# Kernel tuning notes

Measured on AMD Instinct MI355X. Metric: run time of the kernel, lower is better.

## Reference

```python
import jax, jax.numpy as jnp
import numpy as np


def setup_inputs() -> dict:
    key = jax.random.key(0)
    ks = jax.random.split(key, 8)
    B, C, H, W = 4, 512, 64, 64
    M = C // 8
    sq = 1.0 / np.sqrt(C)
    return {
        "x": jax.random.normal(ks[0], (B, C, H, W), jnp.float32),
        "Wq": jax.random.normal(ks[1], (M, C), jnp.float32) * sq,
        "bq": jnp.zeros((M,), jnp.float32),
        "Wk": jax.random.normal(ks[2], (M, C), jnp.float32) * sq,
        "bk": jnp.zeros((M,), jnp.float32),
        "Wv": jax.random.normal(ks[3], (C, C), jnp.float32) * sq,
        "bv": jnp.zeros((C,), jnp.float32),
        "gamma": jax.random.uniform(ks[4], (1,), jnp.float32),
    }


def reference(x, Wq, bq, Wk, bk, Wv, bv, gamma):
    B, C, H, W = x.shape
    N = H * W
    xf = x.reshape(B, C, N)  # flatten spatial -> [B, C, N]
    # 1x1 convs are channel-mixing matmuls
    q = jnp.einsum('mc,bcn->bmn', Wq, xf) + bq[None, :, None]  # [B, M, N]
    k = jnp.einsum('mc,bcn->bmn', Wk, xf) + bk[None, :, None]  # [B, M, N]
    v = jnp.einsum('dc,bcn->bdn', Wv, xf) + bv[None, :, None]  # [B, C, N]
    # sim[b,i,j] = <q[:, i], k[:, j]>, softmax over j
    sim = jnp.einsum('bmi,bmj->bij', q, k)  # [B, N, N]
    attn = jax.nn.softmax(sim, axis=-1)
    # feat[b,c,i] = sum_j v[b,c,j] * attn[b,i,j]
    feat = jnp.einsum('bcj,bij->bci', v, attn)  # [B, C, N]
    out = gamma[0] * feat.reshape(B, C, H, W) + x
    return out
```

## Files before the change

### kernel.cpp

```cpp
#include <hip/hip_runtime.h>

typedef _Float16 f16;
typedef _Float16 f16x8 __attribute__((ext_vector_type(8)));
typedef float    f32x4 __attribute__((ext_vector_type(4)));
typedef unsigned int u32x2 __attribute__((ext_vector_type(2)));

#define B_ 4
#define C_ 512
#define N_ 4096
#define M_ 64

#define LGKM_BARRIER()                                        \
    __builtin_amdgcn_sched_barrier(0);                        \
    asm volatile("s_waitcnt lgkmcnt(0)");                     \
    __builtin_amdgcn_s_barrier();                             \
    __builtin_amdgcn_sched_barrier(0);

__device__ __forceinline__ unsigned pk2(float a, float b) {
    union { f16 h[2]; unsigned u; } t;
    t.h[0] = (f16)a; t.h[1] = (f16)b;
    return t.u;
}

__global__ __launch_bounds__(256) void wcvt(
    const float* __restrict__ Wq, const float* __restrict__ Wk,
    const float* __restrict__ Wv, f16* __restrict__ Wf)
{
    const int e = (blockIdx.x * 256 + threadIdx.x) * 8;
    const float* src;
    int off;
    if (e < 32768)      { src = Wq; off = e; }
    else if (e < 65536) { src = Wk; off = e - 32768; }
    else                { src = Wv; off = e - 65536; }
    float4 a = *(const float4*)(src + off);
    float4 b = *(const float4*)(src + off + 4);
    f16x8 o;
    o[0]=(f16)a.x; o[1]=(f16)a.y; o[2]=(f16)a.z; o[3]=(f16)a.w;
    o[4]=(f16)b.x; o[5]=(f16)b.y; o[6]=(f16)b.z; o[7]=(f16)b.w;
    *(f16x8*)(Wf + e) = o;
}

__global__ __launch_bounds__(512, 2) void qkv4(
    const f16* __restrict__ Wf, const float* __restrict__ x,
    const float* __restrict__ bq, const float* __restrict__ bk,
    const float* __restrict__ bv,
    f16* __restrict__ qt, f16* __restrict__ ktf, f16* __restrict__ vf)
{
    __shared__ __align__(16) char sH[3][8192];
    __shared__ float sBias[640];

    const int tid  = threadIdx.x;
    const int w    = tid >> 6;
    const int lane = tid & 63;
    const int l15  = lane & 15;
    const int quad = lane >> 4;
    const int n0   = blockIdx.x * 64;
    const int b    = blockIdx.y;
    const int row0 = w * 80;

    for (int e = tid; e < 640; e += 512)
        sBias[e] = (e < 64) ? bq[e] : (e < 128) ? bk[e - 64] : bv[e - 128];

    const int wbyte = (lane * 128 + w * 16) ^ ((lane & 7) << 4);
    int rbyte[4][2];
    #pragma unroll
    for (int nt = 0; nt < 4; ++nt)
        #pragma unroll
        for (int kh = 0; kh < 2; ++kh)
            rbyte[nt][kh] = ((nt * 16 + l15) * 128 + kh * 64 + quad * 16)
                            ^ ((l15 & 7) << 4);

    const float* xg = x + (size_t)b * (C_ * N_) + n0 + lane;
    const f16*   wp = Wf + (size_t)row0 * 512 + quad * 8;

    float gn[2][8];
    {
        float g0[8];
        #pragma unroll
        for (int u = 0; u < 8; ++u) g0[u] = xg[(size_t)(w * 8 + u) * N_];
        #pragma unroll
        for (int u = 0; u < 8; ++u) gn[1][u] = xg[(size_t)(64 + w * 8 + u) * N_];
        f16x8 h;
        #pragma unroll
        for (int u = 0; u < 8; ++u) h[u] = (f16)g0[u];
        *(f16x8*)(&sH[0][0] + wbyte) = h;
    }
    LGKM_BARRIER();

    f32x4 acc[5][4] = {};

    #pragma unroll
    for (int t = 0; t < 8; ++t) {
        f16x8 af[5][2];
        #pragma unroll
        for (int ot = 0; ot < 5; ++ot)
            #pragma unroll
            for (int kh = 0; kh < 2; ++kh)
                af[ot][kh] = *(const f16x8*)(wp + (size_t)(ot * 16 + l15) * 512
                                             + t * 64 + kh * 32);
        if (t + 2 < 8) {
            #pragma unroll
            for (int u = 0; u < 8; ++u)
                gn[t & 1][u] = xg[(size_t)((t + 2) * 64 + w * 8 + u) * N_];
        }
        const char* sc = &sH[t % 3][0];
        f16x8 bf[4][2];
        #pragma unroll
        for (int nt = 0; nt < 4; ++nt)
            #pragma unroll
            for (int kh = 0; kh < 2; ++kh)
                bf[nt][kh] = *(const f16x8*)(sc + rbyte[nt][kh]);

        #pragma unroll
        for (int ot = 0; ot < 5; ++ot)
            #pragma unroll
            for (int kh = 0; kh < 2; ++kh)
                #pragma unroll
                for (int nt = 0; nt < 4; ++nt)
                    acc[ot][nt] = __builtin_amdgcn_mfma_f32_16x16x32_f16(
                        af[ot][kh], bf[nt][kh], acc[ot][nt], 0, 0, 0);

        if (t + 1 < 8) {
            f16x8 h;
            #pragma unroll
            for (int u = 0; u < 8; ++u) h[u] = (f16)gn[(t + 1) & 1][u];
            *(f16x8*)(&sH[(t + 1) % 3][0] + wbyte) = h;
        }
        LGKM_BARRIER();
    }

    #pragma unroll
    for (int ot = 0; ot < 5; ++ot) {
        const int rowBase = row0 + ot * 16;
        const int rq = rowBase + quad * 4;
        #pragma unroll
        for (int nt = 0; nt < 4; ++nt) {
            const int n = n0 + nt * 16 + l15;
            union { f16 h[4]; unsigned long long u; } pkv;
            #pragma unroll
            for (int r = 0; r < 4; ++r)
                pkv.h[r] = (f16)(acc[ot][nt][r] + sBias[rq + r]);
            if (rowBase < 64) {
                *(unsigned long long*)(qt + ((size_t)(b * N_ + n)) * M_ + rq) = pkv.u;
            } else if (rowBase < 128) {
                const int ol = rq - 64;
                size_t idx = (((size_t)b * 256 + (n >> 4)) * 2 + (ol >> 5)) * 512
                           + (size_t)((((ol >> 3) & 3) * 16 + (n & 15)) * 8) + (ol & 7);
                *(unsigned long long*)(ktf + idx) = pkv.u;
            } else {
                const int c = rq - 128;
                #pragma unroll
                for (int r = 0; r < 4; ++r) {
                    size_t idx = ((size_t)b * (C_ * N_)) + (size_t)((c + r) >> 4) * 65536
                               + (size_t)(n >> 6) * 1024 + (size_t)((n >> 5) & 1) * 512
                               + (size_t)((((n >> 3) & 3) * 16 + ((c + r) & 15)) * 8) + (n & 7);
                    vf[idx] = pkv.h[r];
                }
            }
        }
    }
}

#define ATTN_BODY(T, CBc, NBc) {                                              \
    f16x8 pbf[4][2];                                                          \
    _Pragma("unroll")                                                         \
    for (int is_ = 0; is_ < 4; ++is_)                                         \
        _Pragma("unroll")                                                     \
        for (int kh_ = 0; kh_ < 2; ++kh_)                                     \
            pbf[is_][kh_] = *(const f16x8*)(pbB + (CBc) * 8192 + rb[is_][kh_]); \
    f32x4 s0 = {}, s1 = {};                                                   \
    s0 = __builtin_amdgcn_mfma_f32_16x16x32_f16(akr[NBc][0], bqf[is0][0], s0, 0, 0, 0); \
    s0 = __builtin_amdgcn_mfma_f32_16x16x32_f16(akr[NBc][1], bqf[is0][1], s0, 0, 0, 0); \
    s1 = __builtin_amdgcn_mfma_f32_16x16x32_f16(akr[NBc][0], bqf[is1][0], s1, 0, 0, 0); \
    s1 = __builtin_amdgcn_mfma_f32_16x16x32_f16(akr[NBc][1], bqf[is1][1], s1, 0, 0, 0); \
    if ((T) + 2 < 64) {                                                       \
        const f16* kn_ = kp + (size_t)((T) + 2) * 4096;                       \
        akr[CBc][0] = *(const f16x8*)(kn_);                                   \
        akr[CBc][1] = *(const f16x8*)(kn_ + 512);                             \
    }                                                                         \
    {                                                                         \
        const f16* vt_ = vln + (size_t)((T) + 1) * 1024;                      \
        _Pragma("unroll")                                                     \
        for (int ct_ = 0; ct_ < 4; ++ct_) {                                   \
            vr[NBc][ct_]     = *(const f16x8*)(vt_ + (size_t)(cw + ct_) * 65536);       \
            vr[NBc][ct_ + 4] = *(const f16x8*)(vt_ + (size_t)(cw + ct_) * 65536 + 512); \
        }                                                                     \
    }                                                                         \
    {                                                                         \
        float p0 = __expf(s0[0] - m0), p1 = __expf(s0[1] - m0);               \
        float p2 = __expf(s0[2] - m0), p3 = __expf(s0[3] - m0);               \
        lp0 += (p0 + p1) + (p2 + p3);                                         \
        u32x2 pw = { pk2(p0, p1), pk2(p2, p3) };                              \
        *(u32x2*)(pbB + (NBc) * 8192 + wb0) = pw;                             \
    }                                                                         \
    {                                                                         \
        float q0 = __expf(s1[0] - m1), q1 = __expf(s1[1] - m1);               \
        float q2 = __expf(s1[2] - m1), q3 = __expf(s1[3] - m1);               \
        lp1 += (q0 + q1) + (q2 + q3);                                         \
        u32x2 pw = { pk2(q0, q1), pk2(q2, q3) };                              \
        *(u32x2*)(pbB + (NBc) * 8192 + wb1) = pw;                             \
    }                                                                         \
    __builtin_amdgcn_s_setprio(1);                                            \
    _Pragma("unroll")                                                         \
    for (int ct_ = 0; ct_ < 4; ++ct_)                                         \
        _Pragma("unroll")                                                     \
        for (int is_ = 0; is_ < 4; ++is_)                                     \
            acc[ct_][is_] = __builtin_amdgcn_mfma_f32_16x16x32_f16(           \
                vr[CBc][ct_], pbf[is_][0], acc[ct_][is_], 0, 0, 0);           \
    _Pragma("unroll")                                                         \
    for (int ct_ = 0; ct_ < 4; ++ct_)                                         \
        _Pragma("unroll")                                                     \
        for (int is_ = 0; is_ < 4; ++is_)                                     \
            acc[ct_][is_] = __builtin_amdgcn_mfma_f32_16x16x32_f16(           \
                vr[CBc][ct_ + 4], pbf[is_][1], acc[ct_][is_], 0, 0, 0);       \
    __builtin_amdgcn_s_setprio(0);                                            \
    LGKM_BARRIER();                                                           \
}

__global__ __launch_bounds__(512, 2) void attn(
    const f16* __restrict__ qt, const f16* __restrict__ ktf,
    const f16* __restrict__ vf, const float* __restrict__ x,
    const float* __restrict__ gamma, float* __restrict__ out)
{
    __shared__ __align__(16) char Pb[2][8192];
    __shared__ float mxs[8][4][16];
    __shared__ float lss[8][4][16];

    const int tid  = threadIdx.x;
    const int w    = tid >> 6;
    const int lane = tid & 63;
    const int l15  = lane & 15;
    const int quad = lane >> 4;
    const int jt   = w & 3;
    const int ish  = w >> 2;
    const int is0  = ish * 2, is1 = is0 + 1;

    const int lin  = blockIdx.x;
    const int b    = (lin & 7) >> 1;
    const int iblk = ((lin >> 3) << 1) | (lin & 1);
    const int i0   = iblk * 64;

    const f16* kln = ktf + (size_t)b * (N_ * M_) + lane * 8;
    const f16* vln = vf  + (size_t)b * (C_ * N_) + lane * 8;

    f16x8 bqf[4][2];
    #pragma unroll
    for (int is = 0; is < 4; ++is)
        #pragma unroll
        for (int kh = 0; kh < 2; ++kh)
            bqf[is][kh] = *(const f16x8*)(qt + ((size_t)(b * N_ + i0 + is * 16 + l15)) * M_
                                          + kh * 32 + quad * 8);

    float mx[4];
    #pragma unroll
    for (int is = 0; is < 4; ++is) mx[is] = -3.0e38f;
    {
        const f16* kw = kln + (size_t)(w * 512) * 64;
        f16x8 akc[4][2];
        #pragma unroll
        for (int t = 0; t < 4; ++t)
            #pragma unroll
            for (int kh = 0; kh < 2; ++kh)
                akc[t][kh] = *(const f16x8*)(kw + t * 1024 + kh * 512);

        #pragma unroll 2
        for (int jj = 0; jj < 512; jj += 64) {
            f16x8 akn[4][2];
            if (jj + 64 < 512) {
                const f16* kn = kw + (size_t)(jj + 64) * 64;
                #pragma unroll
                for (int t = 0; t < 4; ++t)
                    #pragma unroll
                    for (int kh = 0; kh < 2; ++kh)
                        akn[t][kh] = *(const f16x8*)(kn + t * 1024 + kh * 512);
            }
            #pragma unroll
            for (int t = 0; t < 4; ++t) {
                #pragma unroll
                for (int is = 0; is < 4; ++is) {
                    f32x4 s = {};
                    s = __builtin_amdgcn_mfma_f32_16x16x32_f16(akc[t][0], bqf[is][0], s, 0, 0, 0);
                    s = __builtin_amdgcn_mfma_f32_16x16x32_f16(akc[t][1], bqf[is][1], s, 0, 0, 0);
                    mx[is] = fmaxf(mx[is], fmaxf(fmaxf(s[0], s[1]), fmaxf(s[2], s[3])));
                }
            }
            #pragma unroll
            for (int t = 0; t < 4; ++t)
                #pragma unroll
                for (int kh = 0; kh < 2; ++kh)
                    akc[t][kh] = akn[t][kh];
        }
    }
    #pragma unroll
    for (int is = 0; is < 4; ++is) {
        mx[is] = fmaxf(mx[is], __shfl_xor(mx[is], 16, 64));
        mx[is] = fmaxf(mx[is], __shfl_xor(mx[is], 32, 64));
    }
    if (lane < 16) {
        #pragma unroll
        for (int is = 0; is < 4; ++is) mxs[w][is][lane] = mx[is];
    }
    __syncthreads();
    float m0 = -3.0e38f, m1 = -3.0e38f;
    #pragma unroll
    for (int w2 = 0; w2 < 8; ++w2) {
        m0 = fmaxf(m0, mxs[w2][is0][l15]);
        m1 = fmaxf(m1, mxs[w2][is1][l15]);
    }

    f32x4 acc[4][4] = {};
    float lp0 = 0.f, lp1 = 0.f;

    char* pbB = (char*)&Pb[0][0];
    const int swz = (l15 & 7) << 4;
    const int wb0 = ((is0 * 16 + l15) * 128 + (jt * 16 + quad * 4) * 2) ^ swz;
    const int wb1 = wb0 + 2048;
    int rb[4][2];
    #pragma unroll
    for (int is = 0; is < 4; ++is)
        #pragma unroll
        for (int kh = 0; kh < 2; ++kh)
            rb[is][kh] = ((is * 16 + l15) * 128 + kh * 64 + quad * 16) ^ swz;

    const f16* kp = kln + (size_t)(jt * 16) * 64;
    const int cw = w * 4;

    f16x8 akr[2][2];
    f16x8 vr[2][8];

    akr[0][0] = *(const f16x8*)(kp);
    akr[0][1] = *(const f16x8*)(kp + 512);
    {
        f32x4 s0 = {}, s1 = {};
        s0 = __builtin_amdgcn_mfma_f32_16x16x32_f16(akr[0][0], bqf[is0][0], s0, 0, 0, 0);
        s0 = __builtin_amdgcn_mfma_f32_16x16x32_f16(akr[0][1], bqf[is0][1], s0, 0, 0, 0);
        s1 = __builtin_amdgcn_mfma_f32_16x16x32_f16(akr[0][0], bqf[is1][0], s1, 0, 0, 0);
        s1 = __builtin_amdgcn_mfma_f32_16x16x32_f16(akr[0][1], bqf[is1][1], s1, 0, 0, 0);
        float p0 = __expf(s0[0] - m0), p1 = __expf(s0[1] - m0);
        float p2 = __expf(s0[2] - m0), p3 = __expf(s0[3] - m0);
        lp0 += (p0 + p1) + (p2 + p3);
        u32x2 pw0 = { pk2(p0, p1), pk2(p2, p3) };
        *(u32x2*)(pbB + wb0) = pw0;
        float q0 = __expf(s1[0] - m1), q1 = __expf(s1[1] - m1);
        float q2 = __expf(s1[2] - m1), q3 = __expf(s1[3] - m1);
        lp1 += (q0 + q1) + (q2 + q3);
        u32x2 pw1 = { pk2(q0, q1), pk2(q2, q3) };
        *(u32x2*)(pbB + wb1) = pw1;
    }
    akr[1][0] = *(const f16x8*)(kp + 4096);
    akr[1][1] = *(const f16x8*)(kp + 4096 + 512);
    #pragma unroll
    for (int ct = 0; ct < 4; ++ct) {
        vr[0][ct]     = *(const f16x8*)(vln + (size_t)(cw + ct) * 65536);
        vr[0][ct + 4] = *(const f16x8*)(vln + (size_t)(cw + ct) * 65536 + 512);
    }
    __syncthreads();

    for (int tt = 0; tt < 62; tt += 2) {
        ATTN_BODY(tt,     0, 1);
        ATTN_BODY(tt + 1, 1, 0);
    }
    ATTN_BODY(62, 0, 1);

    {
        f16x8 pbf[4][2];
        #pragma unroll
        for (int is = 0; is < 4; ++is)
            #pragma unroll
            for (int kh = 0; kh < 2; ++kh)
                pbf[is][kh] = *(const f16x8*)(pbB + 8192 + rb[is][kh]);
        #pragma unroll
        for (int ct = 0; ct < 4; ++ct)
            #pragma unroll
            for (int is = 0; is < 4; ++is)
                acc[ct][is] = __builtin_amdgcn_mfma_f32_16x16x32_f16(vr[1][ct], pbf[is][0], acc[ct][is], 0, 0, 0);
        #pragma unroll
        for (int ct = 0; ct < 4; ++ct)
            #pragma unroll
            for (int is = 0; is < 4; ++is)
                acc[ct][is] = __builtin_amdgcn_mfma_f32_16x16x32_f16(vr[1][ct + 4], pbf[is][1], acc[ct][is], 0, 0, 0);
    }

    lp0 += __shfl_xor(lp0, 16, 64);
    lp0 += __shfl_xor(lp0, 32, 64);
    lp1 += __shfl_xor(lp1, 16, 64);
    lp1 += __shfl_xor(lp1, 32, 64);
    if (lane < 16) { lss[w][is0][lane] = lp0; lss[w][is1][lane] = lp1; }
    __syncthreads();

    float linv[4];
    #pragma unroll
    for (int is = 0; is < 4; ++is) {
        const int wb = (is >> 1) * 4;
        float l = (lss[wb + 0][is][l15] + lss[wb + 1][is][l15])
                + (lss[wb + 2][is][l15] + lss[wb + 3][is][l15]);
        linv[is] = 1.0f / l;
    }

    const float g = gamma[0];
    #pragma unroll
    for (int is = 0; is < 4; ++is) {
        const int i = i0 + is * 16 + l15;
        #pragma unroll
        for (int ct = 0; ct < 4; ++ct) {
            #pragma unroll
            for (int r = 0; r < 4; ++r) {
                const int c = w * 64 + ct * 16 + quad * 4 + r;
                const size_t idx = ((size_t)(b * C_ + c)) * N_ + i;
                out[idx] = g * (acc[ct][is][r] * linv[is]) + x[idx];
            }
        }
    }
}

extern "C" void kernel_launch(void* const* d_in, const int* in_sizes, int n_in,
                              void* d_out, int out_size, void* d_ws, size_t ws_size,
                              hipStream_t stream)
{
    const float* x     = (const float*)d_in[0];
    const float* Wq    = (const float*)d_in[1];
    const float* bq    = (const float*)d_in[2];
    const float* Wk    = (const float*)d_in[3];
    const float* bk    = (const float*)d_in[4];
    const float* Wv    = (const float*)d_in[5];
    const float* bv    = (const float*)d_in[6];
    const float* gamma = (const float*)d_in[7];
    float* out = (float*)d_out;

    char* ws = (char*)d_ws;
    f16* qt  = (f16*)ws;
    f16* ktf = qt + (size_t)B_ * N_ * M_;
    f16* vf  = ktf + (size_t)B_ * N_ * M_;
    f16* Wf  = vf + (size_t)B_ * C_ * N_;

    wcvt<<<dim3(160), 256, 0, stream>>>(Wq, Wk, Wv, Wf);
    qkv4<<<dim3(N_ / 64, B_), 512, 0, stream>>>(Wf, x, bq, bk, bv, qt, ktf, vf);
    attn<<<dim3(256), 512, 0, stream>>>(qt, ktf, vf, x, gamma, out);
}
```

Measured before the change: 224.8 us.

## Stage full x tile in LDS upfront in QKV projection, drop per-step barriers

The QKV projection kernel now loads the entire 512-channel x tile for its 64 columns into a 64KB swizzled LDS buffer before any compute. This replaces the triple-buffered, software-pipelined stream of 64-channel chunks. All per-iteration barriers in the MFMA loop go away, but global loads no longer overlap with compute and LDS use grows, which may limit occupancy. Both kernels also change their launch bounds to the amdgpu_waves_per_eu(2,2) attribute.

```diff
diff --git a/kernel.cpp b/kernel.cpp
--- a/kernel.cpp
+++ b/kernel.cpp
@@ -40,13 +40,14 @@
     *(f16x8*)(Wf + e) = o;
 }
 
-__global__ __launch_bounds__(512, 2) void qkv4(
+__global__ __launch_bounds__(512) __attribute__((amdgpu_waves_per_eu(2, 2)))
+void qkv5(
     const f16* __restrict__ Wf, const float* __restrict__ x,
     const float* __restrict__ bq, const float* __restrict__ bk,
     const float* __restrict__ bv,
     f16* __restrict__ qt, f16* __restrict__ ktf, f16* __restrict__ vf)
 {
-    __shared__ __align__(16) char sH[3][8192];
+    __shared__ __align__(16) char sX[65536];
     __shared__ float sBias[640];
 
     const int tid  = threadIdx.x;
@@ -61,33 +62,23 @@
     for (int e = tid; e < 640; e += 512)
         sBias[e] = (e < 64) ? bq[e] : (e < 128) ? bk[e - 64] : bv[e - 128];
 
-    const int wbyte = (lane * 128 + w * 16) ^ ((lane & 7) << 4);
-    int rbyte[4][2];
-    #pragma unroll
-    for (int nt = 0; nt < 4; ++nt)
-        #pragma unroll
-        for (int kh = 0; kh < 2; ++kh)
-            rbyte[nt][kh] = ((nt * 16 + l15) * 128 + kh * 64 + quad * 16)
-                            ^ ((l15 & 7) << 4);
-
     const float* xg = x + (size_t)b * (C_ * N_) + n0 + lane;
-    const f16*   wp = Wf + (size_t)row0 * 512 + quad * 8;
-
-    float gn[2][8];
-    {
-        float g0[8];
-        #pragma unroll
-        for (int u = 0; u < 8; ++u) g0[u] = xg[(size_t)(w * 8 + u) * N_];
-        #pragma unroll
-        for (int u = 0; u < 8; ++u) gn[1][u] = xg[(size_t)(64 + w * 8 + u) * N_];
+    #pragma unroll
+    for (int s = 0; s < 8; ++s) {
+        float g[8];
+        #pragma unroll
+        for (int u = 0; u < 8; ++u)
+            g[u] = xg[(size_t)(s * 64 + w * 8 + u) * N_];
         f16x8 h;
         #pragma unroll
-        for (int u = 0; u < 8; ++u) h[u] = (f16)g0[u];
-        *(f16x8*)(&sH[0][0] + wbyte) = h;
-    }
-    LGKM_BARRIER();
+        for (int u = 0; u < 8; ++u) h[u] = (f16)g[u];
+        const int c0 = s * 64 + w * 8;
+        *(f16x8*)(sX + ((lane * 1024 + c0 * 2) ^ ((lane & 7) << 4))) = h;
+    }
+    __syncthreads();
 
     f32x4 acc[5][4] = {};
+    const f16* wp = Wf + (size_t)row0 * 512 + quad * 8;
 
     #pragma unroll
     for (int t = 0; t < 8; ++t) {
@@ -98,18 +89,15 @@
             for (int kh = 0; kh < 2; ++kh)
                 af[ot][kh] = *(const f16x8*)(wp + (size_t)(ot * 16 + l15) * 512
                                              + t * 64 + kh * 32);
-        if (t + 2 < 8) {
-            #pragma unroll
-            for (int u = 0; u < 8; ++u)
-                gn[t & 1][u] = xg[(size_t)((t + 2) * 64 + w * 8 + u) * N_];
-        }
-        const char* sc = &sH[t % 3][0];
         f16x8 bf[4][2];
         #pragma unroll
         for (int nt = 0; nt < 4; ++nt)
             #pragma unroll
-            for (int kh = 0; kh < 2; ++kh)
-                bf[nt][kh] = *(const f16x8*)(sc + rbyte[nt][kh]);
+            for (int kh = 0; kh < 2; ++kh) {
+                const int byte = ((nt * 16 + l15) * 1024 + t * 128 + kh * 64 + quad * 16)
+                                 ^ ((l15 & 7) << 4);
+                bf[nt][kh] = *(const f16x8*)(sX + byte);
+            }
 
         #pragma unroll
         for (int ot = 0; ot < 5; ++ot)
@@ -119,14 +107,6 @@
                 for (int nt = 0; nt < 4; ++nt)
                     acc[ot][nt] = __builtin_amdgcn_mfma_f32_16x16x32_f16(
                         af[ot][kh], bf[nt][kh], acc[ot][nt], 0, 0, 0);
-
-        if (t + 1 < 8) {
-            f16x8 h;
-            #pragma unroll
-            for (int u = 0; u < 8; ++u) h[u] = (f16)gn[(t + 1) & 1][u];
-            *(f16x8*)(&sH[(t + 1) % 3][0] + wbyte) = h;
-        }
-        LGKM_BARRIER();
     }
 
     #pragma unroll
@@ -217,7 +197,8 @@
     LGKM_BARRIER();                                                           \
 }
 
-__global__ __launch_bounds__(512, 2) void attn(
+__global__ __launch_bounds__(512) __attribute__((amdgpu_waves_per_eu(2, 2)))
+void attn(
     const f16* __restrict__ qt, const f16* __restrict__ ktf,
     const f16* __restrict__ vf, const float* __restrict__ x,
     const float* __restrict__ gamma, float* __restrict__ out)
@@ -434,6 +415,6 @@
     f16* Wf  = vf + (size_t)B_ * C_ * N_;
 
     wcvt<<<dim3(160), 256, 0, stream>>>(Wq, Wk, Wv, Wf);
-    qkv4<<<dim3(N_ / 64, B_), 512, 0, stream>>>(Wf, x, bq, bk, bv, qt, ktf, vf);
+    qkv5<<<dim3(N_ / 64, B_), 512, 0, stream>>>(Wf, x, bq, bk, bv, qt, ktf, vf);
     attn<<<dim3(256), 512, 0, stream>>>(qt, ktf, vf, x, gamma, out);
 }
```

New measurement: 219.4 us. 1.02x faster.
